# Performance work log

Measured on AMD Instinct MI355X. Metric: run time of the kernel, lower is better.

The kernel has to match this reference:

```python
import jax, jax.numpy as jnp
import numpy as np

N = 16384
E = 524288
D_IN = 128
D_OUT = 128


def setup_inputs() -> dict:
    key = jax.random.key(0)
    k1, k2, k3 = jax.random.split(key, 3)
    x = jax.random.normal(k1, (N, D_IN), dtype=jnp.float32)
    edge_index = jax.random.randint(k2, (2, E), 0, N, dtype=jnp.int64)
    # Xavier-uniform init for weight (matches nn.init.xavier_uniform_)
    limit = float(np.sqrt(6.0 / (D_IN + D_OUT)))
    weight = jax.random.uniform(k3, (D_IN, D_OUT), dtype=jnp.float32,
                                minval=-limit, maxval=limit)
    return {"x": x, "edge_index": edge_index, "num_nodes": N, "weight": weight}


def reference(x, edge_index, num_nodes, weight):
    # Dense symmetric 0/1 adjacency via index set (faithful to the torch code)
    adj = jnp.zeros((num_nodes, num_nodes), dtype=jnp.float32)
    adj = adj.at[edge_index[0], edge_index[1]].set(1.0)
    adj = adj.at[edge_index[1], edge_index[0]].set(1.0)
    h = x @ weight            # [N, D_out]
    h = adj @ h               # [N, D_out] aggregation
    return jax.nn.relu(h)
```

## Files before the change

kernel.cpp:

```cpp
#include <hip/hip_runtime.h>
#include <hip/hip_bf16.h>
#include <cstdint>
#include <cstddef>


constexpr int NN   = 16384;
constexpr int D    = 128;
constexpr int NB   = 512;
constexpr int RPB  = 32;
constexpr int WPR  = NN / 32;
constexpr int EPB  = 4096;
constexpr int SLOT = 48;
constexpr int LCAP = 320;

constexpr size_t H2_OFF  = 262144;
constexpr size_t ENT_OFF = H2_OFF + (size_t)NN * 64 * 4;

__device__ inline unsigned short f2bf(float f) {
    union { float f; unsigned int u; } x; x.f = f;
    unsigned int u = x.u;
    unsigned int r = (u + 0x7fffu + ((u >> 16) & 1u)) >> 16;
    return (unsigned short)r;
}

__global__ __launch_bounds__(256) void part_gemm_kernel(
    const int* __restrict__ ei, int E, int nPart,
    unsigned int* __restrict__ counts, unsigned int* __restrict__ entries,
    const float* __restrict__ x, const float* __restrict__ w,
    unsigned int* __restrict__ h2) {
    __shared__ __align__(16) char smem[65536];
    const int tid = threadIdx.x;

    if ((int)blockIdx.x < nPart) {
        int* loff = (int*)smem;
        for (int i = tid; i < NB; i += 256) loff[i] = 0;
        __syncthreads();

        const int e0 = blockIdx.x * EPB;
        const int pb = blockIdx.x;
        #pragma unroll
        for (int k = 0; k < 16; ++k) {
            int p = e0 + k * 256 + tid;
            if (p < E) {
                int u = ei[p];
                int v = ei[E + p];
                int b1 = u >> 5;
                int o1 = atomicAdd(&loff[b1], 1);
                if (o1 < SLOT)
                    entries[((size_t)b1 * nPart + pb) * SLOT + o1] =
                        ((unsigned)(u & 31) << 14) | (unsigned)v;
                int b2 = v >> 5;
                int o2 = atomicAdd(&loff[b2], 1);
                if (o2 < SLOT)
                    entries[((size_t)b2 * nPart + pb) * SLOT + o2] =
                        ((unsigned)(v & 31) << 14) | (unsigned)u;
            }
        }
        __syncthreads();
        for (int b = tid; b < NB; b += 256) {
            int c = loff[b]; if (c > SLOT) c = SLOT;
            counts[(size_t)b * nPart + pb] = (unsigned)c;
        }
        return;
    }

    float (*xt)[64] = (float(*)[64])smem;
    float (*wl)[64] = (float(*)[64])(smem + 32768);
    const int gb   = (int)blockIdx.x - nPart;
    const int rb   = gb >> 1, cb = gb & 1;
    const int row0 = rb * 64, col0 = cb * 64;

    for (int i = tid; i < 64 * (D / 4); i += 256) {
        int r = i >> 5, k4 = i & 31;
        float4 xv = *(const float4*)&x[(size_t)(row0 + r) * D + (k4 << 2)];
        xt[(k4 << 2) + 0][r] = xv.x;
        xt[(k4 << 2) + 1][r] = xv.y;
        xt[(k4 << 2) + 2][r] = xv.z;
        xt[(k4 << 2) + 3][r] = xv.w;
    }
    for (int i = tid; i < D * (64 / 4); i += 256) {
        int k = i >> 4, c4 = i & 15;
        *(float4*)&wl[k][c4 << 2] =
            *(const float4*)&w[(size_t)k * D + col0 + (c4 << 2)];
    }
    __syncthreads();

    const int cg = tid & 15, rg = tid >> 4;
    const int c0 = cg << 2, r0 = rg << 2;
    float acc[4][4] = {};
    #pragma unroll 4
    for (int k = 0; k < D; ++k) {
        float4 xv = *(float4*)&xt[k][r0];
        float4 wv = *(float4*)&wl[k][c0];
        const float xr[4] = {xv.x, xv.y, xv.z, xv.w};
        const float wc[4] = {wv.x, wv.y, wv.z, wv.w};
        #pragma unroll
        for (int r = 0; r < 4; ++r)
            #pragma unroll
            for (int c = 0; c < 4; ++c)
                acc[r][c] = fmaf(xr[r], wc[c], acc[r][c]);
    }
    #pragma unroll
    for (int r = 0; r < 4; ++r) {
        unsigned int p0 = (unsigned int)f2bf(acc[r][0]) |
                          ((unsigned int)f2bf(acc[r][1]) << 16);
        unsigned int p1 = (unsigned int)f2bf(acc[r][2]) |
                          ((unsigned int)f2bf(acc[r][3]) << 16);
        uint2 vv; vv.x = p0; vv.y = p1;
        *(uint2*)&h2[(size_t)(row0 + r0 + r) * 64 + ((col0 + c0) >> 1)] = vv;
    }
}

__global__ __launch_bounds__(512) void agg_kernel(
    const unsigned int* __restrict__ counts, int nPart,
    const unsigned int* __restrict__ entries,
    const unsigned int* __restrict__ h2, float* __restrict__ out) {
    __shared__ unsigned int mask[RPB * WPR];
    __shared__ int cnt_s[128];
    __shared__ int Lw[8][LCAP];
    const int b = blockIdx.x, tid = threadIdx.x;
    const int wave = tid >> 6, lane = tid & 63;

    for (int i = tid; i < RPB * WPR; i += 512) mask[i] = 0;
    if (tid < nPart) {
        int c = (int)counts[(size_t)b * nPart + tid];
        if (c > SLOT) c = SLOT;
        cnt_s[tid] = c;
    }
    __syncthreads();

    const int segs = nPart >> 3;
    for (int s = wave * segs; s < (wave + 1) * segs && s < nPart; ++s) {
        int c = cnt_s[s];
        if (lane < c) {
            unsigned int e = entries[((size_t)b * nPart + s) * SLOT + lane];
            unsigned int lr = e >> 14, cc = e & 16383u;
            atomicOr(&mask[lr * WPR + (cc >> 5)], 1u << (cc & 31u));
        }
    }
    __syncthreads();

    const int r0 = b * RPB;
    for (int rr = wave; rr < RPB; rr += 8) {
        const unsigned int* mrow = &mask[rr * WPR];
        unsigned int wbits[8];
        int c = 0;
        #pragma unroll
        for (int k = 0; k < 8; ++k) {
            wbits[k] = mrow[lane + k * 64];
            c += __popc(wbits[k]);
        }
        int inc = c;
        #pragma unroll
        for (int dd = 1; dd < 64; dd <<= 1) {
            int t = __shfl_up(inc, dd);
            if (lane >= dd) inc += t;
        }
        int p = inc - c;
        int total = __shfl(inc, 63);
        if (total > LCAP) total = LCAP;
        int* L = Lw[wave];
        #pragma unroll
        for (int k = 0; k < 8; ++k) {
            unsigned int m = wbits[k];
            int cbase = (lane + k * 64) << 5;
            while (m) {
                int bt = __builtin_ctz(m);
                m &= m - 1;
                if (p < LCAP) L[p] = cbase + bt;
                ++p;
            }
        }
        asm volatile("s_waitcnt lgkmcnt(0)" ::: "memory");

        float a0 = 0.f, a1 = 0.f;
        int i = 0;
        for (; i + 8 <= total; i += 8) {
            unsigned int u0 = h2[(unsigned)L[i + 0] * 64u + lane];
            unsigned int u1 = h2[(unsigned)L[i + 1] * 64u + lane];
            unsigned int u2 = h2[(unsigned)L[i + 2] * 64u + lane];
            unsigned int u3 = h2[(unsigned)L[i + 3] * 64u + lane];
            unsigned int u4 = h2[(unsigned)L[i + 4] * 64u + lane];
            unsigned int u5 = h2[(unsigned)L[i + 5] * 64u + lane];
            unsigned int u6 = h2[(unsigned)L[i + 6] * 64u + lane];
            unsigned int u7 = h2[(unsigned)L[i + 7] * 64u + lane];
            a0 += __uint_as_float(u0 << 16); a1 += __uint_as_float(u0 & 0xffff0000u);
            a0 += __uint_as_float(u1 << 16); a1 += __uint_as_float(u1 & 0xffff0000u);
            a0 += __uint_as_float(u2 << 16); a1 += __uint_as_float(u2 & 0xffff0000u);
            a0 += __uint_as_float(u3 << 16); a1 += __uint_as_float(u3 & 0xffff0000u);
            a0 += __uint_as_float(u4 << 16); a1 += __uint_as_float(u4 & 0xffff0000u);
            a0 += __uint_as_float(u5 << 16); a1 += __uint_as_float(u5 & 0xffff0000u);
            a0 += __uint_as_float(u6 << 16); a1 += __uint_as_float(u6 & 0xffff0000u);
            a0 += __uint_as_float(u7 << 16); a1 += __uint_as_float(u7 & 0xffff0000u);
        }
        for (; i < total; ++i) {
            unsigned int u0 = h2[(unsigned)L[i] * 64u + lane];
            a0 += __uint_as_float(u0 << 16); a1 += __uint_as_float(u0 & 0xffff0000u);
        }
        float2 r; r.x = fmaxf(a0, 0.f); r.y = fmaxf(a1, 0.f);
        *(float2*)&out[(size_t)(r0 + rr) * D + lane * 2] = r;
    }
}

extern "C" void kernel_launch(void* const* d_in, const int* in_sizes, int n_in,
                              void* d_out, int out_size, void* d_ws, size_t ws_size,
                              hipStream_t stream) {
    const float* x  = (const float*)d_in[0];
    const int*   ei = (const int*)d_in[1];
    const float* w  = (const float*)d_in[3];
    float* out = (float*)d_out;

    unsigned int* counts  = (unsigned int*)d_ws;
    unsigned int* h2      = (unsigned int*)((char*)d_ws + H2_OFF);
    unsigned int* entries = (unsigned int*)((char*)d_ws + ENT_OFF);

    const int E = in_sizes[1] / 2;
    const int nPart = (E + EPB - 1) / EPB;

    part_gemm_kernel<<<nPart + 512, 256, 0, stream>>>(
        ei, E, nPart, counts, entries, x, w, h2);
    agg_kernel<<<NB, 512, 0, stream>>>(counts, nPart, entries, h2, out);
}
```

Before: 64.94 us.

## Compute x@W with bf16 MFMA instead of FP32 FMA outer product

Replaces the scalar FP32 register-tiled GEMM with bf16 MFMA 16x16x32 instructions. Inputs are converted to bf16 while being staged into XOR-swizzled shared memory, which also halves the LDS footprint. The aim is to cut the GEMM blocks' compute time and free LDS for occupancy. In exchange, x and W are rounded to bf16 before the multiply rather than only the output, and the output is now written as scattered 2-byte stores.

```diff
diff --git a/kernel.cpp b/kernel.cpp
--- a/kernel.cpp
+++ b/kernel.cpp
@@ -16,6 +16,9 @@
 constexpr size_t H2_OFF  = 262144;
 constexpr size_t ENT_OFF = H2_OFF + (size_t)NN * 64 * 4;
 
+typedef short short8 __attribute__((ext_vector_type(8)));
+typedef float f32x4  __attribute__((ext_vector_type(4)));
+
 __device__ inline unsigned short f2bf(float f) {
     union { float f; unsigned int u; } x; x.f = f;
     unsigned int u = x.u;
@@ -27,8 +30,8 @@
     const int* __restrict__ ei, int E, int nPart,
     unsigned int* __restrict__ counts, unsigned int* __restrict__ entries,
     const float* __restrict__ x, const float* __restrict__ w,
-    unsigned int* __restrict__ h2) {
-    __shared__ __align__(16) char smem[65536];
+    unsigned short* __restrict__ h2s) {
+    __shared__ __align__(16) char smem[32768];
     const int tid = threadIdx.x;
 
     if ((int)blockIdx.x < nPart) {
@@ -64,51 +67,75 @@
         return;
     }
 
-    float (*xt)[64] = (float(*)[64])smem;
-    float (*wl)[64] = (float(*)[64])(smem + 32768);
     const int gb   = (int)blockIdx.x - nPart;
     const int rb   = gb >> 1, cb = gb & 1;
     const int row0 = rb * 64, col0 = cb * 64;
 
-    for (int i = tid; i < 64 * (D / 4); i += 256) {
-        int r = i >> 5, k4 = i & 31;
-        float4 xv = *(const float4*)&x[(size_t)(row0 + r) * D + (k4 << 2)];
-        xt[(k4 << 2) + 0][r] = xv.x;
-        xt[(k4 << 2) + 1][r] = xv.y;
-        xt[(k4 << 2) + 2][r] = xv.z;
-        xt[(k4 << 2) + 3][r] = xv.w;
-    }
-    for (int i = tid; i < D * (64 / 4); i += 256) {
-        int k = i >> 4, c4 = i & 15;
-        *(float4*)&wl[k][c4 << 2] =
-            *(const float4*)&w[(size_t)k * D + col0 + (c4 << 2)];
+    #pragma unroll
+    for (int j = 0; j < 8; ++j) {
+        int f  = tid + j * 256;
+        int r  = f >> 5, c4 = f & 31;
+        float4 xv = *(const float4*)&x[(size_t)(row0 + r) * D + (c4 << 2)];
+        unsigned int lo = (unsigned)f2bf(xv.x) | ((unsigned)f2bf(xv.y) << 16);
+        unsigned int hi = (unsigned)f2bf(xv.z) | ((unsigned)f2bf(xv.w) << 16);
+        int g = c4 >> 1;
+        int byte = r * 256 + ((g ^ (r & 7)) << 4) + ((c4 & 1) << 3);
+        uint2 p; p.x = lo; p.y = hi;
+        *(uint2*)&smem[byte] = p;
+    }
+    #pragma unroll
+    for (int j = 0; j < 8; ++j) {
+        int f  = tid + j * 256;
+        int k  = f >> 4, c4 = f & 15;
+        float4 wv = *(const float4*)&w[(size_t)k * D + col0 + (c4 << 2)];
+        const float vals[4] = {wv.x, wv.y, wv.z, wv.w};
+        #pragma unroll
+        for (int i = 0; i < 4; ++i) {
+            int c = (c4 << 2) + i;
+            int byte = 16384 + c * 256 + (((k >> 3) ^ (c & 7)) << 4) + ((k & 7) << 1);
+            *(unsigned short*)&smem[byte] = f2bf(vals[i]);
+        }
     }
     __syncthreads();
 
-    const int cg = tid & 15, rg = tid >> 4;
-    const int c0 = cg << 2, r0 = rg << 2;
-    float acc[4][4] = {};
-    #pragma unroll 4
-    for (int k = 0; k < D; ++k) {
-        float4 xv = *(float4*)&xt[k][r0];
-        float4 wv = *(float4*)&wl[k][c0];
-        const float xr[4] = {xv.x, xv.y, xv.z, xv.w};
-        const float wc[4] = {wv.x, wv.y, wv.z, wv.w};
-        #pragma unroll
-        for (int r = 0; r < 4; ++r)
+    const int lane = tid & 63, wave = tid >> 6;
+    const int wr = wave >> 1, wc = wave & 1;
+    const int l15 = lane & 15, l4 = lane >> 4;
+
+    f32x4 acc[2][2] = {};
+    #pragma unroll
+    for (int kk = 0; kk < 4; ++kk) {
+        int g = (kk << 2) + l4;
+        short8 a[2], b[2];
+        #pragma unroll
+        for (int mi = 0; mi < 2; ++mi) {
+            int r = wr * 32 + mi * 16 + l15;
+            a[mi] = *(short8*)&smem[r * 256 + ((g ^ (r & 7)) << 4)];
+        }
+        #pragma unroll
+        for (int ni = 0; ni < 2; ++ni) {
+            int c = wc * 32 + ni * 16 + l15;
+            b[ni] = *(short8*)&smem[16384 + c * 256 + ((g ^ (c & 7)) << 4)];
+        }
+        #pragma unroll
+        for (int mi = 0; mi < 2; ++mi)
             #pragma unroll
-            for (int c = 0; c < 4; ++c)
-                acc[r][c] = fmaf(xr[r], wc[c], acc[r][c]);
-    }
-    #pragma unroll
-    for (int r = 0; r < 4; ++r) {
-        unsigned int p0 = (unsigned int)f2bf(acc[r][0]) |
-                          ((unsigned int)f2bf(acc[r][1]) << 16);
-        unsigned int p1 = (unsigned int)f2bf(acc[r][2]) |
-                          ((unsigned int)f2bf(acc[r][3]) << 16);
-        uint2 vv; vv.x = p0; vv.y = p1;
-        *(uint2*)&h2[(size_t)(row0 + r0 + r) * 64 + ((col0 + c0) >> 1)] = vv;
-    }
+            for (int ni = 0; ni < 2; ++ni)
+                acc[mi][ni] = __builtin_amdgcn_mfma_f32_16x16x32_bf16(
+                    a[mi], b[ni], acc[mi][ni], 0, 0, 0);
+    }
+
+    #pragma unroll
+    for (int mi = 0; mi < 2; ++mi)
+        #pragma unroll
+        for (int ni = 0; ni < 2; ++ni) {
+            int col = col0 + wc * 32 + ni * 16 + l15;
+            #pragma unroll
+            for (int reg = 0; reg < 4; ++reg) {
+                int row = row0 + wr * 32 + mi * 16 + (l4 << 2) + reg;
+                h2s[(size_t)row * D + col] = f2bf(acc[mi][ni][reg]);
+            }
+        }
 }
 
 __global__ __launch_bounds__(512) void agg_kernel(
@@ -210,14 +237,15 @@
     const float* w  = (const float*)d_in[3];
     float* out = (float*)d_out;
 
-    unsigned int* counts  = (unsigned int*)d_ws;
-    unsigned int* h2      = (unsigned int*)((char*)d_ws + H2_OFF);
-    unsigned int* entries = (unsigned int*)((char*)d_ws + ENT_OFF);
+    unsigned int*   counts  = (unsigned int*)d_ws;
+    unsigned short* h2s     = (unsigned short*)((char*)d_ws + H2_OFF);
+    unsigned int*   h2      = (unsigned int*)((char*)d_ws + H2_OFF);
+    unsigned int*   entries = (unsigned int*)((char*)d_ws + ENT_OFF);
 
     const int E = in_sizes[1] / 2;
     const int nPart = (E + EPB - 1) / EPB;
 
     part_gemm_kernel<<<nPart + 512, 256, 0, stream>>>(
-        ei, E, nPart, counts, entries, x, w, h2);
+        ei, E, nPart, counts, entries, x, w, h2s);
     agg_kernel<<<NB, 512, 0, stream>>>(counts, nPart, entries, h2, out);
 }
```

Measured after the change: 59.09 us. -9.0%, faster.
